# Performance work log

Hardware: AMD Instinct MI355X
Metric: run time of the kernel (lower is better)

## Reference

```python
import jax, jax.numpy as jnp
import numpy as np

N_NODES = 100000
N_EDGES = 1600000
D_FEAT = 64


def setup_inputs() -> dict:
    key = jax.random.key(0)
    k1, k2 = jax.random.split(key)
    x = jax.random.normal(k1, (N_NODES, D_FEAT), dtype=jnp.float32)
    edge_index = jax.random.randint(k2, (2, N_EDGES), 0, N_NODES, dtype=jnp.int64)
    alpha = jnp.ones((), dtype=jnp.float32)
    res_scale = jnp.ones((), dtype=jnp.float32)
    return {"x": x, "alpha": alpha, "res_scale": res_scale, "edge_index": edge_index}


def reference(x, alpha, res_scale, edge_index):
    """LGConv (symmetric gcn_norm, no self-loops) -> alpha-scale -> residual.

    out_i = alpha * sum_{(j->i) in E} x_j / sqrt(deg_i * deg_j) + res_scale * x_i
    """
    n = x.shape[0]
    row, col = edge_index[0], edge_index[1]  # source, target
    # degree from target index (as in PyG gcn_norm with add_self_loops=False)
    deg = jax.ops.segment_sum(jnp.ones(row.shape[0], dtype=x.dtype), col, num_segments=n)
    deg_inv_sqrt = jnp.where(deg > 0, jax.lax.rsqrt(jnp.maximum(deg, 1.0)), 0.0)
    norm = deg_inv_sqrt[row] * deg_inv_sqrt[col]  # (E,)
    msgs = norm[:, None] * x[row]                  # (E, d) gather + scale
    out = jax.ops.segment_sum(msgs, col, num_segments=n)  # scatter-add to targets
    return alpha * out + res_scale * x
```

## Files before the change

### kernel.cpp

```cpp
#include <hip/hip_runtime.h>
#include <hip/hip_bf16.h>

#define D_FEAT 64
#define OVF_CAP 65536
#define EB 4096
#define NBMAX 1024

typedef unsigned int uint32;

__device__ inline float blo(uint32 u) { return __uint_as_float(u << 16); }
__device__ inline float bhi(uint32 u) { return __uint_as_float(u & 0xffff0000u); }
__device__ inline float dinv(int d) { return (d > 0) ? rsqrtf((float)d) : 0.0f; }

__global__ __launch_bounds__(1024) void k_scatter(const int* __restrict__ row,
                                                  const int* __restrict__ col,
                                                  const float2* __restrict__ x2,
                                                  uint32* __restrict__ xb,
                                                  int* __restrict__ deg,
                                                  int* __restrict__ cursor,
                                                  uint32* __restrict__ binned,
                                                  int* __restrict__ slots,
                                                  int2* __restrict__ ovf,
                                                  int* __restrict__ ovf_cnt,
                                                  int nhalf, int E, int nb,
                                                  int CAP, int C) {
    __shared__ int h[NBMAX];
    for (int i = threadIdx.x; i < nb; i += 1024) h[i] = 0;
    __syncthreads();
    const int s = blockIdx.x * EB;
    const int e = (s + EB < E) ? s + EB : E;
    for (int i = s + threadIdx.x; i < e; i += 1024)
        atomicAdd(&h[col[i] >> 7], 1);
    __syncthreads();
    for (int k = threadIdx.x; k < nb; k += 1024) {
        int c = h[k];
        if (c) h[k] = atomicAdd(&cursor[k], c);
    }
    __syncthreads();
    for (int i = s + threadIdx.x; i < e; i += 1024) {
        int c = col[i];
        uint32 r = (uint32)row[i];
        int b = c >> 7;
        int pos = atomicAdd(&h[b], 1);
        if (pos < CAP) {
            binned[(size_t)b * CAP + pos] = (r << 7) | (uint32)(c & 127);
        } else {
            int rk = atomicAdd(&deg[c], 1);
            if (rk < C) {
                slots[(size_t)c * C + rk] = (int)r;
            } else {
                int o = atomicAdd(ovf_cnt, 1);
                if (o < OVF_CAP) ovf[o] = make_int2((int)r, c);
            }
        }
    }
    const int t = blockIdx.x * 1024 + threadIdx.x;
    const int stride = gridDim.x * 1024;
    for (int j = t; j < nhalf; j += stride) {
        float2 v = x2[j];
        __hip_bfloat16 bx = __float2bfloat16(v.x);
        __hip_bfloat16 by = __float2bfloat16(v.y);
        uint32 ux = *reinterpret_cast<unsigned short*>(&bx);
        uint32 uy = *reinterpret_cast<unsigned short*>(&by);
        xb[j] = ux | (uy << 16);
    }
}

__global__ __launch_bounds__(512) void k_build(const int* __restrict__ cursor,
                                               const uint32* __restrict__ binned,
                                               int* __restrict__ slots,
                                               int* __restrict__ deg,
                                               float* __restrict__ winv,
                                               int2* __restrict__ ovf,
                                               int* __restrict__ ovf_cnt,
                                               int n, int C, int CAP) {
    __shared__ int cnt[128];
    const int k = blockIdx.x;
    const int base = k << 7;
    if (threadIdx.x < 128) {
        int node = base + threadIdx.x;
        cnt[threadIdx.x] = (node < n) ? deg[node] : 0;
    }
    __syncthreads();
    int tot = cursor[k];
    const int e = (tot < CAP) ? tot : CAP;
    const uint32* seg = binned + (size_t)k * CAP;
    for (int i = threadIdx.x; i < e; i += 512) {
        uint32 pk = seg[i];
        int cl = (int)(pk & 127);
        int r  = (int)(pk >> 7);
        int rk = atomicAdd(&cnt[cl], 1);
        if (rk < C) {
            slots[(size_t)(base + cl) * C + rk] = r;
        } else {
            int o = atomicAdd(ovf_cnt, 1);
            if (o < OVF_CAP) ovf[o] = make_int2(r, base + cl);
        }
    }
    __syncthreads();
    int i = base + threadIdx.x;
    if (threadIdx.x < 128 && i < n) {
        int d = cnt[threadIdx.x];
        deg[i] = d;
        winv[i] = dinv(d);
    }
}

__global__ void k_gather4d(const uint32* __restrict__ xb,
                           const float4* __restrict__ x4,
                           const int* __restrict__ deg,
                           const float* __restrict__ winv,
                           const int* __restrict__ slots,
                           const float* __restrict__ alpha_p,
                           const float* __restrict__ rs_p,
                           float4* __restrict__ out4, int n, int C) {
    int wid = (blockIdx.x * blockDim.x + threadIdx.x) >> 6;
    if (wid >= n) return;
    const int lane = threadIdx.x & 63;
    const int q = lane >> 4;
    const int l = lane & 15;
    int d = deg[wid];
    int e = (d < C) ? d : C;
    float4 xr = make_float4(0.f, 0.f, 0.f, 0.f);
    if (q == 0) xr = x4[(size_t)wid * 16 + l];
    const int* sl = slots + (size_t)wid * C;
    float ax = 0.f, ay = 0.f, az = 0.f, aw = 0.f;
    int k = 0;
    for (; k + 16 <= e; k += 16) {
        int s0 = sl[k + q];
        int s1 = sl[k + 4 + q];
        int s2 = sl[k + 8 + q];
        int s3 = sl[k + 12 + q];
        float w0 = winv[s0], w1 = winv[s1], w2 = winv[s2], w3 = winv[s3];
        uint2 p0 = ((const uint2*)(xb + (size_t)s0 * 32))[l];
        uint2 p1 = ((const uint2*)(xb + (size_t)s1 * 32))[l];
        uint2 p2 = ((const uint2*)(xb + (size_t)s2 * 32))[l];
        uint2 p3 = ((const uint2*)(xb + (size_t)s3 * 32))[l];
        ax = fmaf(w0, blo(p0.x), ax); ay = fmaf(w0, bhi(p0.x), ay);
        az = fmaf(w0, blo(p0.y), az); aw = fmaf(w0, bhi(p0.y), aw);
        ax = fmaf(w1, blo(p1.x), ax); ay = fmaf(w1, bhi(p1.x), ay);
        az = fmaf(w1, blo(p1.y), az); aw = fmaf(w1, bhi(p1.y), aw);
        ax = fmaf(w2, blo(p2.x), ax); ay = fmaf(w2, bhi(p2.x), ay);
        az = fmaf(w2, blo(p2.y), az); aw = fmaf(w2, bhi(p2.y), aw);
        ax = fmaf(w3, blo(p3.x), ax); ay = fmaf(w3, bhi(p3.x), ay);
        az = fmaf(w3, blo(p3.y), az); aw = fmaf(w3, bhi(p3.y), aw);
    }
    for (; k < e; k += 4) {
        int kk = k + q;
        if (kk < e) {
            int s0 = sl[kk];
            float w0 = winv[s0];
            uint2 p0 = ((const uint2*)(xb + (size_t)s0 * 32))[l];
            ax = fmaf(w0, blo(p0.x), ax); ay = fmaf(w0, bhi(p0.x), ay);
            az = fmaf(w0, blo(p0.y), az); aw = fmaf(w0, bhi(p0.y), aw);
        }
    }
    ax += __shfl_down(ax, 32, 64); ay += __shfl_down(ay, 32, 64);
    az += __shfl_down(az, 32, 64); aw += __shfl_down(aw, 32, 64);
    ax += __shfl_down(ax, 16, 64); ay += __shfl_down(ay, 16, 64);
    az += __shfl_down(az, 16, 64); aw += __shfl_down(aw, 16, 64);
    if (q == 0) {
        float adw = (*alpha_p) * winv[wid];
        float rs  = *rs_p;
        float4 o;
        o.x = fmaf(adw, ax, rs * xr.x);
        o.y = fmaf(adw, ay, rs * xr.y);
        o.z = fmaf(adw, az, rs * xr.z);
        o.w = fmaf(adw, aw, rs * xr.w);
        out4[(size_t)wid * 16 + l] = o;
    }
}

__global__ void k_ovf(const int2* __restrict__ ovf, const int* __restrict__ cnt_p,
                      const float* __restrict__ x, const float* __restrict__ winv,
                      const float* __restrict__ alpha_p, float* __restrict__ out) {
    int cnt = *cnt_p;
    if (cnt > OVF_CAP) cnt = OVF_CAP;
    if (cnt <= 0) return;
    float a = *alpha_p;
    long long total = (long long)cnt * 64;
    long long stride = (long long)gridDim.x * blockDim.x;
    for (long long idx = blockIdx.x * (long long)blockDim.x + threadIdx.x;
         idx < total; idx += stride) {
        int e = (int)(idx >> 6);
        int f = (int)(idx & 63);
        int2 rc = ovf[e];
        float w = a * winv[rc.x] * winv[rc.y];
        atomicAdd(&out[(size_t)rc.y * D_FEAT + f], w * x[(size_t)rc.x * D_FEAT + f]);
    }
}

__global__ void k_winv(const int* __restrict__ deg, float* __restrict__ winv, int n) {
    int i = blockIdx.x * blockDim.x + threadIdx.x;
    if (i < n) winv[i] = dinv(deg[i]);
}

__global__ __launch_bounds__(256) void k_prep(const float2* __restrict__ x2,
                                              uint32* __restrict__ xb,
                                              const int* __restrict__ row,
                                              const int* __restrict__ col,
                                              int* __restrict__ deg,
                                              int* __restrict__ slots,
                                              int2* __restrict__ ovf,
                                              int* __restrict__ ovf_cnt,
                                              int nhalf, int E, int C) {
    const int t = blockIdx.x * blockDim.x + threadIdx.x;
    if (t < E) {
        int c = col[t];
        int r = row[t];
        int rk = atomicAdd(&deg[c], 1);
        if (rk < C) {
            slots[(size_t)c * C + rk] = r;
        } else {
            int o = atomicAdd(ovf_cnt, 1);
            if (o < OVF_CAP) ovf[o] = make_int2(r, c);
        }
    }
    const int stride = gridDim.x * blockDim.x;
    for (int j = t; j < nhalf; j += stride) {
        float2 v = x2[j];
        __hip_bfloat16 bx = __float2bfloat16(v.x);
        __hip_bfloat16 by = __float2bfloat16(v.y);
        uint32 ux = *reinterpret_cast<unsigned short*>(&bx);
        uint32 uy = *reinterpret_cast<unsigned short*>(&by);
        xb[j] = ux | (uy << 16);
    }
}

static inline char* align_up(char* p, size_t a) {
    return (char*)(((uintptr_t)p + (a - 1)) & ~(uintptr_t)(a - 1));
}

extern "C" void kernel_launch(void* const* d_in, const int* in_sizes, int n_in,
                              void* d_out, int out_size, void* d_ws, size_t ws_size,
                              hipStream_t stream) {
    const float* x         = (const float*)d_in[0];
    const float* alpha     = (const float*)d_in[1];
    const float* res_scale = (const float*)d_in[2];
    const int*   ei        = (const int*)d_in[3];

    const int n = in_sizes[0] / D_FEAT;
    const int E = in_sizes[3] / 2;
    const int* row = ei;
    const int* col = ei + E;

    float* out = (float*)d_out;
    const int nhalf = n * (D_FEAT / 2);
    const int nb = (n + 127) >> 7;
    const int B  = (E + EB - 1) / EB;
    const int C  = 32;

    {
        char* p = (char*)d_ws;
        int*    deg     = (int*)p;            p += (size_t)n * 4;
        int*    cursor  = (int*)p;            p += (size_t)nb * 4;
        int*    ovf_cnt = (int*)p;            p += 4;
        float*  winv    = (float*)p;          p += (size_t)n * 4;
        int2*   ovf     = (int2*)p;           p += (size_t)OVF_CAP * 8;
        p = align_up(p, 16);
        uint32* xb      = (uint32*)p;         p += (size_t)n * 128;
        int*    slots   = (int*)p;            p += (size_t)n * C * 4;
        p = align_up(p, 16);
        uint32* binned  = (uint32*)p;
        const size_t fixed = (size_t)((char*)binned - (char*)d_ws);

        int CAP = 0;
        if (ws_size > fixed) {
            long long avail = (long long)(ws_size - fixed) / ((long long)nb * 4);
            CAP = (avail > 4096) ? 4096 : (int)avail;
            CAP &= ~31;
        }
        const bool ok = (CAP >= 1600) && (nb <= NBMAX) && (n <= (NBMAX << 7));
        if (ok) {
            hipMemsetAsync(deg, 0, (size_t)(n + nb + 1) * 4, stream);
            k_scatter<<<B, 1024, 0, stream>>>(row, col, (const float2*)x, xb,
                                              deg, cursor, binned, slots,
                                              ovf, ovf_cnt, nhalf, E, nb, CAP, C);
            k_build<<<nb, 512, 0, stream>>>(cursor, binned, slots, deg, winv,
                                            ovf, ovf_cnt, n, C, CAP);
            const long long tt = (long long)n * D_FEAT;
            const int blocks = (int)((tt + 255) / 256);
            k_gather4d<<<blocks, 256, 0, stream>>>(xb, (const float4*)x, deg, winv,
                                                   slots, alpha, res_scale,
                                                   (float4*)out, n, C);
            k_ovf<<<64, 256, 0, stream>>>(ovf, ovf_cnt, x, winv, alpha, out);
            return;
        }
    }

    {
        char* q = (char*)d_ws;
        int*    degf    = (int*)q;            q += (size_t)n * 4;
        int*    ovf_cf  = (int*)q;            q += 4;
        float*  winvf   = (float*)q;          q += (size_t)n * 4;
        int2*   ovff    = (int2*)q;           q += (size_t)OVF_CAP * 8;
        q = align_up(q, 16);
        uint32* xbf     = (uint32*)q;         q += (size_t)n * 128;
        int*    slotsf  = (int*)q;
        const size_t fxd = (size_t)(q - (char*)d_ws);
        int Cf = 0;
        if (ws_size > fxd) {
            size_t c_avail = (ws_size - fxd) / ((size_t)n * 4);
            Cf = (c_avail > 32) ? 32 : (int)c_avail;
        }
        if (Cf < 1) return;
        hipMemsetAsync(degf, 0, (size_t)n * 4 + 4, stream);
        k_prep<<<(E + 255) / 256, 256, 0, stream>>>(
            (const float2*)x, xbf, row, col, degf, slotsf, ovff, ovf_cf,
            nhalf, E, Cf);
        k_winv<<<(n + 255) / 256, 256, 0, stream>>>(degf, winvf, n);
        const long long tt = (long long)n * D_FEAT;
        const int blocks = (int)((tt + 255) / 256);
        k_gather4d<<<blocks, 256, 0, stream>>>(xbf, (const float4*)x, degf, winvf,
                                               slotsf, alpha, res_scale,
                                               (float4*)out, n, Cf);
        k_ovf<<<64, 256, 0, stream>>>(ovff, ovf_cf, x, winvf, alpha, out);
    }
}
```

Measured before the change: 182.4 us.

## Fuse scatter, build and gather into one cooperative kernel with LDS slot lists

Replaces the separate scatter, build and gather kernels with one cooperative kernel that uses grid-wide syncs between phases. Each block owns 128 target nodes and keeps their neighbor slot lists in shared memory rather than a global slots array, which removes the global slot writes and reads and two kernel launches. Binning now runs on only 256 blocks with larger edge chunks. The cost is grid.sync overhead, occupancy limited to one block per 128 nodes (782 blocks), and lower parallelism in the binning phase.

```diff
diff --git a/kernel.cpp b/kernel.cpp
--- a/kernel.cpp
+++ b/kernel.cpp
@@ -1,10 +1,14 @@
 #include <hip/hip_runtime.h>
 #include <hip/hip_bf16.h>
+#include <hip/hip_cooperative_groups.h>
+
+namespace cg = cooperative_groups;
 
 #define D_FEAT 64
 #define OVF_CAP 65536
-#define EB 4096
+#define NBIN 256
 #define NBMAX 1024
+#define CSLOT 32
 
 typedef unsigned int uint32;
 
@@ -12,50 +16,201 @@
 __device__ inline float bhi(uint32 u) { return __uint_as_float(u & 0xffff0000u); }
 __device__ inline float dinv(int d) { return (d > 0) ? rsqrtf((float)d) : 0.0f; }
 
-__global__ __launch_bounds__(1024) void k_scatter(const int* __restrict__ row,
-                                                  const int* __restrict__ col,
-                                                  const float2* __restrict__ x2,
-                                                  uint32* __restrict__ xb,
-                                                  int* __restrict__ deg,
-                                                  int* __restrict__ cursor,
-                                                  uint32* __restrict__ binned,
-                                                  int* __restrict__ slots,
-                                                  int2* __restrict__ ovf,
-                                                  int* __restrict__ ovf_cnt,
-                                                  int nhalf, int E, int nb,
-                                                  int CAP, int C) {
-    __shared__ int h[NBMAX];
-    for (int i = threadIdx.x; i < nb; i += 1024) h[i] = 0;
-    __syncthreads();
-    const int s = blockIdx.x * EB;
-    const int e = (s + EB < E) ? s + EB : E;
-    for (int i = s + threadIdx.x; i < e; i += 1024)
-        atomicAdd(&h[col[i] >> 7], 1);
-    __syncthreads();
-    for (int k = threadIdx.x; k < nb; k += 1024) {
-        int c = h[k];
-        if (c) h[k] = atomicAdd(&cursor[k], c);
-    }
-    __syncthreads();
-    for (int i = s + threadIdx.x; i < e; i += 1024) {
-        int c = col[i];
-        uint32 r = (uint32)row[i];
-        int b = c >> 7;
-        int pos = atomicAdd(&h[b], 1);
-        if (pos < CAP) {
-            binned[(size_t)b * CAP + pos] = (r << 7) | (uint32)(c & 127);
-        } else {
-            int rk = atomicAdd(&deg[c], 1);
-            if (rk < C) {
-                slots[(size_t)c * C + rk] = (int)r;
+__global__ __launch_bounds__(512, 8) void k_coop(
+    const int* __restrict__ row, const int* __restrict__ col,
+    const float2* __restrict__ x2, uint32* __restrict__ xb,
+    int* __restrict__ deg, float* __restrict__ winv,
+    int* __restrict__ cursor, uint32* __restrict__ binned,
+    int2* __restrict__ ovf, int* __restrict__ ovf_cnt,
+    const float* __restrict__ alpha_p, const float* __restrict__ rs_p,
+    const float4* __restrict__ x4, float4* __restrict__ out4,
+    int n, int E, int nb, int CAP, int EB2, int nhalf)
+{
+    __shared__ int   slots[128 * CSLOT];
+    __shared__ int   cnt[128];
+    __shared__ float winvl[128];
+    const int bid = blockIdx.x;
+    const int tid = threadIdx.x;
+    cg::grid_group grid = cg::this_grid();
+
+    if (bid < NBIN) {
+        int* h = slots;
+        for (int i = tid; i < nb; i += 512) h[i] = 0;
+        __syncthreads();
+        const int s = bid * EB2;
+        const int e = (s + EB2 < E) ? s + EB2 : E;
+        for (int i = s + tid; i < e; i += 512)
+            atomicAdd(&h[col[i] >> 7], 1);
+        __syncthreads();
+        for (int k = tid; k < nb; k += 512) {
+            int c = h[k];
+            if (c) h[k] = atomicAdd(&cursor[k], c);
+        }
+        __syncthreads();
+        for (int i = s + tid; i < e; i += 512) {
+            int c = col[i];
+            uint32 r = (uint32)row[i];
+            int b = c >> 7;
+            int pos = atomicAdd(&h[b], 1);
+            if (pos < CAP) {
+                binned[(size_t)b * CAP + pos] = (r << 7) | (uint32)(c & 127);
             } else {
+                atomicAdd(&deg[c], 1);
                 int o = atomicAdd(ovf_cnt, 1);
                 if (o < OVF_CAP) ovf[o] = make_int2((int)r, c);
             }
         }
     }
-    const int t = blockIdx.x * 1024 + threadIdx.x;
-    const int stride = gridDim.x * 1024;
+    for (int j = bid * 512 + tid; j < nhalf; j += nb * 512) {
+        float2 v = x2[j];
+        __hip_bfloat16 bx = __float2bfloat16(v.x);
+        __hip_bfloat16 by = __float2bfloat16(v.y);
+        uint32 ux = *reinterpret_cast<unsigned short*>(&bx);
+        uint32 uy = *reinterpret_cast<unsigned short*>(&by);
+        xb[j] = ux | (uy << 16);
+    }
+    grid.sync();
+
+    if (tid < 128) cnt[tid] = 0;
+    __syncthreads();
+    const int base = bid << 7;
+    int tot = cursor[bid];
+    if (tot > CAP) tot = CAP;
+    const uint32* seg = binned + (size_t)bid * CAP;
+    for (int i = tid; i < tot; i += 512) {
+        uint32 pk = seg[i];
+        int cl = (int)(pk & 127);
+        int r  = (int)(pk >> 7);
+        int rk = atomicAdd(&cnt[cl], 1);
+        if (rk < CSLOT) {
+            slots[(cl << 5) + rk] = r;
+        } else {
+            int o = atomicAdd(ovf_cnt, 1);
+            if (o < OVF_CAP) ovf[o] = make_int2(r, base + cl);
+        }
+    }
+    __syncthreads();
+    if (tid < 128) {
+        int node = base + tid;
+        if (node < n) {
+            int d = cnt[tid] + deg[node];
+            deg[node] = d;
+            float w = dinv(d);
+            winv[node] = w;
+            winvl[tid] = w;
+        } else {
+            winvl[tid] = 0.f;
+        }
+    }
+    grid.sync();
+
+    const int wv   = tid >> 6;
+    const int lane = tid & 63;
+    const int q = lane >> 4;
+    const int l = lane & 15;
+    const float alpha = *alpha_p;
+    const float rs = *rs_p;
+    for (int nl = (wv << 4); nl < (wv << 4) + 16; ++nl) {
+        int node = base + nl;
+        if (node >= n) break;
+        int e = cnt[nl];
+        if (e > CSLOT) e = CSLOT;
+        float4 xr = make_float4(0.f, 0.f, 0.f, 0.f);
+        if (q == 0) xr = x4[(size_t)node * 16 + l];
+        const int* sl = &slots[nl << 5];
+        float ax = 0.f, ay = 0.f, az = 0.f, aw = 0.f;
+        int k = 0;
+        for (; k + 16 <= e; k += 16) {
+            int s0 = sl[k + q];
+            int s1 = sl[k + 4 + q];
+            int s2 = sl[k + 8 + q];
+            int s3 = sl[k + 12 + q];
+            float w0 = winv[s0], w1 = winv[s1], w2 = winv[s2], w3 = winv[s3];
+            uint2 p0 = ((const uint2*)(xb + (size_t)s0 * 32))[l];
+            uint2 p1 = ((const uint2*)(xb + (size_t)s1 * 32))[l];
+            uint2 p2 = ((const uint2*)(xb + (size_t)s2 * 32))[l];
+            uint2 p3 = ((const uint2*)(xb + (size_t)s3 * 32))[l];
+            ax = fmaf(w0, blo(p0.x), ax); ay = fmaf(w0, bhi(p0.x), ay);
+            az = fmaf(w0, blo(p0.y), az); aw = fmaf(w0, bhi(p0.y), aw);
+            ax = fmaf(w1, blo(p1.x), ax); ay = fmaf(w1, bhi(p1.x), ay);
+            az = fmaf(w1, blo(p1.y), az); aw = fmaf(w1, bhi(p1.y), aw);
+            ax = fmaf(w2, blo(p2.x), ax); ay = fmaf(w2, bhi(p2.x), ay);
+            az = fmaf(w2, blo(p2.y), az); aw = fmaf(w2, bhi(p2.y), aw);
+            ax = fmaf(w3, blo(p3.x), ax); ay = fmaf(w3, bhi(p3.x), ay);
+            az = fmaf(w3, blo(p3.y), az); aw = fmaf(w3, bhi(p3.y), aw);
+        }
+        for (; k < e; k += 4) {
+            int kk = k + q;
+            if (kk < e) {
+                int s0 = sl[kk];
+                float w0 = winv[s0];
+                uint2 p0 = ((const uint2*)(xb + (size_t)s0 * 32))[l];
+                ax = fmaf(w0, blo(p0.x), ax); ay = fmaf(w0, bhi(p0.x), ay);
+                az = fmaf(w0, blo(p0.y), az); aw = fmaf(w0, bhi(p0.y), aw);
+            }
+        }
+        ax += __shfl_down(ax, 32, 64); ay += __shfl_down(ay, 32, 64);
+        az += __shfl_down(az, 32, 64); aw += __shfl_down(aw, 32, 64);
+        ax += __shfl_down(ax, 16, 64); ay += __shfl_down(ay, 16, 64);
+        az += __shfl_down(az, 16, 64); aw += __shfl_down(aw, 16, 64);
+        if (q == 0) {
+            float adw = alpha * winvl[nl];
+            float4 o;
+            o.x = fmaf(adw, ax, rs * xr.x);
+            o.y = fmaf(adw, ay, rs * xr.y);
+            o.z = fmaf(adw, az, rs * xr.z);
+            o.w = fmaf(adw, aw, rs * xr.w);
+            out4[(size_t)node * 16 + l] = o;
+        }
+    }
+}
+
+__global__ void k_ovf(const int2* __restrict__ ovf, const int* __restrict__ cnt_p,
+                      const float* __restrict__ x, const float* __restrict__ winv,
+                      const float* __restrict__ alpha_p, float* __restrict__ out) {
+    int cnt = *cnt_p;
+    if (cnt > OVF_CAP) cnt = OVF_CAP;
+    if (cnt <= 0) return;
+    float a = *alpha_p;
+    long long total = (long long)cnt * 64;
+    long long stride = (long long)gridDim.x * blockDim.x;
+    for (long long idx = blockIdx.x * (long long)blockDim.x + threadIdx.x;
+         idx < total; idx += stride) {
+        int e = (int)(idx >> 6);
+        int f = (int)(idx & 63);
+        int2 rc = ovf[e];
+        float w = a * winv[rc.x] * winv[rc.y];
+        atomicAdd(&out[(size_t)rc.y * D_FEAT + f], w * x[(size_t)rc.x * D_FEAT + f]);
+    }
+}
+
+__global__ void k_winv(const int* __restrict__ deg, float* __restrict__ winv, int n) {
+    int i = blockIdx.x * blockDim.x + threadIdx.x;
+    if (i < n) winv[i] = dinv(deg[i]);
+}
+
+__global__ __launch_bounds__(256) void k_prep(const float2* __restrict__ x2,
+                                              uint32* __restrict__ xb,
+                                              const int* __restrict__ row,
+                                              const int* __restrict__ col,
+                                              int* __restrict__ deg,
+                                              int* __restrict__ slots,
+                                              int2* __restrict__ ovf,
+                                              int* __restrict__ ovf_cnt,
+                                              int nhalf, int E, int C) {
+    const int t = blockIdx.x * blockDim.x + threadIdx.x;
+    if (t < E) {
+        int c = col[t];
+        int r = row[t];
+        int rk = atomicAdd(&deg[c], 1);
+        if (rk < C) {
+            slots[(size_t)c * C + rk] = r;
+        } else {
+            int o = atomicAdd(ovf_cnt, 1);
+            if (o < OVF_CAP) ovf[o] = make_int2(r, c);
+        }
+    }
+    const int stride = gridDim.x * blockDim.x;
     for (int j = t; j < nhalf; j += stride) {
         float2 v = x2[j];
         __hip_bfloat16 bx = __float2bfloat16(v.x);
@@ -63,46 +218,6 @@
         uint32 ux = *reinterpret_cast<unsigned short*>(&bx);
         uint32 uy = *reinterpret_cast<unsigned short*>(&by);
         xb[j] = ux | (uy << 16);
-    }
-}
-
-__global__ __launch_bounds__(512) void k_build(const int* __restrict__ cursor,
-                                               const uint32* __restrict__ binned,
-                                               int* __restrict__ slots,
-                                               int* __restrict__ deg,
-                                               float* __restrict__ winv,
-                                               int2* __restrict__ ovf,
-                                               int* __restrict__ ovf_cnt,
-                                               int n, int C, int CAP) {
-    __shared__ int cnt[128];
-    const int k = blockIdx.x;
-    const int base = k << 7;
-    if (threadIdx.x < 128) {
-        int node = base + threadIdx.x;
-        cnt[threadIdx.x] = (node < n) ? deg[node] : 0;
-    }
-    __syncthreads();
-    int tot = cursor[k];
-    const int e = (tot < CAP) ? tot : CAP;
-    const uint32* seg = binned + (size_t)k * CAP;
-    for (int i = threadIdx.x; i < e; i += 512) {
-        uint32 pk = seg[i];
-        int cl = (int)(pk & 127);
-        int r  = (int)(pk >> 7);
-        int rk = atomicAdd(&cnt[cl], 1);
-        if (rk < C) {
-            slots[(size_t)(base + cl) * C + rk] = r;
-        } else {
-            int o = atomicAdd(ovf_cnt, 1);
-            if (o < OVF_CAP) ovf[o] = make_int2(r, base + cl);
-        }
-    }
-    __syncthreads();
-    int i = base + threadIdx.x;
-    if (threadIdx.x < 128 && i < n) {
-        int d = cnt[threadIdx.x];
-        deg[i] = d;
-        winv[i] = dinv(d);
     }
 }
 
@@ -171,62 +286,6 @@
     }
 }
 
-__global__ void k_ovf(const int2* __restrict__ ovf, const int* __restrict__ cnt_p,
-                      const float* __restrict__ x, const float* __restrict__ winv,
-                      const float* __restrict__ alpha_p, float* __restrict__ out) {
-    int cnt = *cnt_p;
-    if (cnt > OVF_CAP) cnt = OVF_CAP;
-    if (cnt <= 0) return;
-    float a = *alpha_p;
-    long long total = (long long)cnt * 64;
-    long long stride = (long long)gridDim.x * blockDim.x;
-    for (long long idx = blockIdx.x * (long long)blockDim.x + threadIdx.x;
-         idx < total; idx += stride) {
-        int e = (int)(idx >> 6);
-        int f = (int)(idx & 63);
-        int2 rc = ovf[e];
-        float w = a * winv[rc.x] * winv[rc.y];
-        atomicAdd(&out[(size_t)rc.y * D_FEAT + f], w * x[(size_t)rc.x * D_FEAT + f]);
-    }
-}
-
-__global__ void k_winv(const int* __restrict__ deg, float* __restrict__ winv, int n) {
-    int i = blockIdx.x * blockDim.x + threadIdx.x;
-    if (i < n) winv[i] = dinv(deg[i]);
-}
-
-__global__ __launch_bounds__(256) void k_prep(const float2* __restrict__ x2,
-                                              uint32* __restrict__ xb,
-                                              const int* __restrict__ row,
-                                              const int* __restrict__ col,
-                                              int* __restrict__ deg,
-                                              int* __restrict__ slots,
-                                              int2* __restrict__ ovf,
-                                              int* __restrict__ ovf_cnt,
-                                              int nhalf, int E, int C) {
-    const int t = blockIdx.x * blockDim.x + threadIdx.x;
-    if (t < E) {
-        int c = col[t];
-        int r = row[t];
-        int rk = atomicAdd(&deg[c], 1);
-        if (rk < C) {
-            slots[(size_t)c * C + rk] = r;
-        } else {
-            int o = atomicAdd(ovf_cnt, 1);
-            if (o < OVF_CAP) ovf[o] = make_int2(r, c);
-        }
-    }
-    const int stride = gridDim.x * blockDim.x;
-    for (int j = t; j < nhalf; j += stride) {
-        float2 v = x2[j];
-        __hip_bfloat16 bx = __float2bfloat16(v.x);
-        __hip_bfloat16 by = __float2bfloat16(v.y);
-        uint32 ux = *reinterpret_cast<unsigned short*>(&bx);
-        uint32 uy = *reinterpret_cast<unsigned short*>(&by);
-        xb[j] = ux | (uy << 16);
-    }
-}
-
 static inline char* align_up(char* p, size_t a) {
     return (char*)(((uintptr_t)p + (a - 1)) & ~(uintptr_t)(a - 1));
 }
@@ -247,8 +306,7 @@
     float* out = (float*)d_out;
     const int nhalf = n * (D_FEAT / 2);
     const int nb = (n + 127) >> 7;
-    const int B  = (E + EB - 1) / EB;
-    const int C  = 32;
+    const int EB2 = (E + NBIN - 1) / NBIN;
 
     {
         char* p = (char*)d_ws;
@@ -259,7 +317,6 @@
         int2*   ovf     = (int2*)p;           p += (size_t)OVF_CAP * 8;
         p = align_up(p, 16);
         uint32* xb      = (uint32*)p;         p += (size_t)n * 128;
-        int*    slots   = (int*)p;            p += (size_t)n * C * 4;
         p = align_up(p, 16);
         uint32* binned  = (uint32*)p;
         const size_t fixed = (size_t)((char*)binned - (char*)d_ws);
@@ -270,21 +327,44 @@
             CAP = (avail > 4096) ? 4096 : (int)avail;
             CAP &= ~31;
         }
-        const bool ok = (CAP >= 1600) && (nb <= NBMAX) && (n <= (NBMAX << 7));
+
+        static int coop_cap = -1;
+        if (coop_cap < 0) {
+            int perCU = 0, nCU = 0, dev = 0;
+            hipGetDevice(&dev);
+            if (hipOccupancyMaxActiveBlocksPerMultiprocessor(&perCU, k_coop,
+                                                             512, 0) != hipSuccess)
+                perCU = 0;
+            if (hipDeviceGetAttribute(&nCU, hipDeviceAttributeMultiprocessorCount,
+                                      dev) != hipSuccess)
+                nCU = 0;
+            coop_cap = perCU * nCU;
+        }
+
+        const bool ok = (CAP >= 2560) && (nb <= NBMAX) && (nb <= coop_cap);
         if (ok) {
             hipMemsetAsync(deg, 0, (size_t)(n + nb + 1) * 4, stream);
-            k_scatter<<<B, 1024, 0, stream>>>(row, col, (const float2*)x, xb,
-                                              deg, cursor, binned, slots,
-                                              ovf, ovf_cnt, nhalf, E, nb, CAP, C);
-            k_build<<<nb, 512, 0, stream>>>(cursor, binned, slots, deg, winv,
-                                            ovf, ovf_cnt, n, C, CAP);
-            const long long tt = (long long)n * D_FEAT;
-            const int blocks = (int)((tt + 255) / 256);
-            k_gather4d<<<blocks, 256, 0, stream>>>(xb, (const float4*)x, deg, winv,
-                                                   slots, alpha, res_scale,
-                                                   (float4*)out, n, C);
-            k_ovf<<<64, 256, 0, stream>>>(ovf, ovf_cnt, x, winv, alpha, out);
-            return;
+            const int*    row_a = row;      const int*   col_a = col;
+            const float2* x2_a  = (const float2*)x;
+            uint32*       xb_a  = xb;       int*         deg_a = deg;
+            float*        wv_a  = winv;     int*         cur_a = cursor;
+            uint32*       bin_a = binned;   int2*        ovf_a = ovf;
+            int*          ovc_a = ovf_cnt;
+            const float*  al_a  = alpha;    const float* rs_a  = res_scale;
+            const float4* x4_a  = (const float4*)x;
+            float4*       out_a = (float4*)out;
+            int n_a = n, E_a = E, nb_a = nb, CAP_a = CAP, EB2_a = EB2,
+                nh_a = nhalf;
+            void* args[] = { &row_a, &col_a, &x2_a, &xb_a, &deg_a, &wv_a,
+                             &cur_a, &bin_a, &ovf_a, &ovc_a, &al_a, &rs_a,
+                             &x4_a, &out_a, &n_a, &E_a, &nb_a, &CAP_a,
+                             &EB2_a, &nh_a };
+            hipError_t err = hipLaunchCooperativeKernel(
+                (const void*)k_coop, dim3(nb), dim3(512), args, 0, stream);
+            if (err == hipSuccess) {
+                k_ovf<<<64, 256, 0, stream>>>(ovf, ovf_cnt, x, winv, alpha, out);
+                return;
+            }
         }
     }
 
```

Result: slower. 247.3 us (+35.6%).

## Replace atomic binning with two-pass ballot-based radix partition and in-place slot ranking

Applied to the files above, without the earlier changes.

The one-pass scatter kernel used per-edge shared-memory atomics to sort edges into 128-node bins. It is replaced by a two-level radix partition: first by 4096-node range, then into 32 sub-bins. Each level uses wave ballot and popcount prefix sums instead of atomics. A rank kernel stages each bin in LDS and writes per-node slot lists back into the binned buffer in place, so the separate slots array is gone. The range buffer reuses the bf16 x storage before it is written. This adds an extra kernel pass and heavy unrolled ballot loops over 32 buckets. It also depends on tight capacity assumptions such as n ≤ 131072 and the per-bin cap CAPB.

```diff
diff --git a/kernel.cpp b/kernel.cpp
--- a/kernel.cpp
+++ b/kernel.cpp
@@ -3,106 +3,219 @@
 
 #define D_FEAT 64
 #define OVF_CAP 65536
-#define EB 4096
-#define NBMAX 1024
+#define NRMAX 32
+#define RS_EB 2048
+#define NCH 16
+#define CAPB 4096
+#define CSL 32
 
 typedef unsigned int uint32;
+typedef unsigned long long ull;
 
 __device__ inline float blo(uint32 u) { return __uint_as_float(u << 16); }
 __device__ inline float bhi(uint32 u) { return __uint_as_float(u & 0xffff0000u); }
 __device__ inline float dinv(int d) { return (d > 0) ? rsqrtf((float)d) : 0.0f; }
 
-__global__ __launch_bounds__(1024) void k_scatter(const int* __restrict__ row,
-                                                  const int* __restrict__ col,
-                                                  const float2* __restrict__ x2,
-                                                  uint32* __restrict__ xb,
-                                                  int* __restrict__ deg,
-                                                  int* __restrict__ cursor,
-                                                  uint32* __restrict__ binned,
-                                                  int* __restrict__ slots,
-                                                  int2* __restrict__ ovf,
-                                                  int* __restrict__ ovf_cnt,
-                                                  int nhalf, int E, int nb,
-                                                  int CAP, int C) {
-    __shared__ int h[NBMAX];
-    for (int i = threadIdx.x; i < nb; i += 1024) h[i] = 0;
+__global__ __launch_bounds__(256) void k_rsplit(const int* __restrict__ row,
+                                                const int* __restrict__ col,
+                                                uint32* __restrict__ rseg,
+                                                int* __restrict__ rcur,
+                                                int* __restrict__ deg,
+                                                int2* __restrict__ ovf,
+                                                int* __restrict__ ovf_cnt,
+                                                int E, int nr, int RCAP) {
+    __shared__ int wcnt[4][NRMAX];
+    __shared__ int wbase[4][NRMAX];
+    const int wv = threadIdx.x >> 6;
+    const int lane = threadIdx.x & 63;
+    const ull mlt = ((ull)1 << lane) - 1;
+    const int s = blockIdx.x * RS_EB;
+
+    int cnt[NRMAX];
+#pragma unroll
+    for (int k = 0; k < NRMAX; ++k) cnt[k] = 0;
+#pragma unroll
+    for (int it = 0; it < RS_EB / 256; ++it) {
+        int i = s + it * 256 + wv * 64 + lane;
+        int b = 63;
+        if (i < E) b = col[i] >> 12;
+#pragma unroll
+        for (int k = 0; k < NRMAX; ++k)
+            cnt[k] += __popcll(__ballot(b == k));
+    }
+    if (lane == 0) {
+#pragma unroll
+        for (int k = 0; k < NRMAX; ++k) wcnt[wv][k] = cnt[k];
+    }
     __syncthreads();
-    const int s = blockIdx.x * EB;
-    const int e = (s + EB < E) ? s + EB : E;
-    for (int i = s + threadIdx.x; i < e; i += 1024)
-        atomicAdd(&h[col[i] >> 7], 1);
+    if (threadIdx.x < NRMAX) {
+        int k = threadIdx.x;
+        int t0 = wcnt[0][k], t1 = wcnt[1][k], t2 = wcnt[2][k], t3 = wcnt[3][k];
+        int tot = t0 + t1 + t2 + t3;
+        int g = tot ? atomicAdd(&rcur[k], tot) : 0;
+        wbase[0][k] = g;
+        wbase[1][k] = g + t0;
+        wbase[2][k] = g + t0 + t1;
+        wbase[3][k] = g + t0 + t1 + t2;
+    }
     __syncthreads();
-    for (int k = threadIdx.x; k < nb; k += 1024) {
-        int c = h[k];
-        if (c) h[k] = atomicAdd(&cursor[k], c);
-    }
+    int run[NRMAX];
+#pragma unroll
+    for (int k = 0; k < NRMAX; ++k) run[k] = wbase[wv][k];
+#pragma unroll
+    for (int it = 0; it < RS_EB / 256; ++it) {
+        int i = s + it * 256 + wv * 64 + lane;
+        int b = 63, c = 0, r = 0;
+        if (i < E) { c = col[i]; r = row[i]; b = c >> 12; }
+#pragma unroll
+        for (int k = 0; k < NRMAX; ++k) {
+            ull m = __ballot(b == k);
+            if (b == k) {
+                int pos = run[k] + __popcll(m & mlt);
+                if (pos < RCAP) {
+                    rseg[(size_t)k * RCAP + pos] =
+                        ((uint32)r << 12) | (uint32)(c & 4095);
+                } else {
+                    atomicAdd(&deg[c], 1);
+                    int o = atomicAdd(ovf_cnt, 1);
+                    if (o < OVF_CAP) ovf[o] = make_int2(r, c);
+                }
+            }
+            run[k] += __popcll(m);
+        }
+    }
+}
+
+__global__ __launch_bounds__(512) void k_bsplit(const uint32* __restrict__ rseg,
+                                                const int* __restrict__ rcur,
+                                                uint32* __restrict__ binned,
+                                                int* __restrict__ cursor,
+                                                int* __restrict__ deg,
+                                                int2* __restrict__ ovf,
+                                                int* __restrict__ ovf_cnt,
+                                                int nr, int RCAP) {
+    __shared__ int wcnt[8][32];
+    __shared__ int wbase[8][32];
+    const int rg = blockIdx.x & 31;
+    if (rg >= nr) return;
+    int len = rcur[rg];
+    if (len > RCAP) len = RCAP;
+    const uint32* sg = rseg + (size_t)rg * RCAP;
+    const int wv = threadIdx.x >> 6;
+    const int lane = threadIdx.x & 63;
+    const ull mlt = ((ull)1 << lane) - 1;
+
+    for (int c0 = (blockIdx.x >> 5) * 4096; c0 < len; c0 += NCH * 4096) {
+        const int cend = (c0 + 4096 < len) ? c0 + 4096 : len;
+        int cnt[32];
+#pragma unroll
+        for (int k = 0; k < 32; ++k) cnt[k] = 0;
+#pragma unroll
+        for (int it = 0; it < 8; ++it) {
+            int i = c0 + it * 512 + wv * 64 + lane;
+            int b = 63;
+            if (i < cend) b = (int)((sg[i] >> 7) & 31);
+#pragma unroll
+            for (int k = 0; k < 32; ++k)
+                cnt[k] += __popcll(__ballot(b == k));
+        }
+        if (lane == 0) {
+#pragma unroll
+            for (int k = 0; k < 32; ++k) wcnt[wv][k] = cnt[k];
+        }
+        __syncthreads();
+        if (threadIdx.x < 32) {
+            int k = threadIdx.x;
+            int tot = 0, acc;
+            int t[8];
+#pragma unroll
+            for (int w = 0; w < 8; ++w) { t[w] = wcnt[w][k]; tot += t[w]; }
+            int g = tot ? atomicAdd(&cursor[(rg << 5) + k], tot) : 0;
+            acc = g;
+#pragma unroll
+            for (int w = 0; w < 8; ++w) { wbase[w][k] = acc; acc += t[w]; }
+        }
+        __syncthreads();
+        int run[32];
+#pragma unroll
+        for (int k = 0; k < 32; ++k) run[k] = wbase[wv][k];
+#pragma unroll
+        for (int it = 0; it < 8; ++it) {
+            int i = c0 + it * 512 + wv * 64 + lane;
+            int b = 63;
+            uint32 v = 0;
+            if (i < cend) { v = sg[i]; b = (int)((v >> 7) & 31); }
+#pragma unroll
+            for (int k = 0; k < 32; ++k) {
+                ull m = __ballot(b == k);
+                if (b == k) {
+                    int pos = run[k] + __popcll(m & mlt);
+                    int bk = (rg << 5) + k;
+                    if (pos < CAPB) {
+                        binned[(size_t)bk * CAPB + pos] =
+                            ((v >> 12) << 7) | (v & 127u);
+                    } else {
+                        int cf = (rg << 12) + (int)(v & 4095u);
+                        atomicAdd(&deg[cf], 1);
+                        int o = atomicAdd(ovf_cnt, 1);
+                        if (o < OVF_CAP) ovf[o] = make_int2((int)(v >> 12), cf);
+                    }
+                }
+                run[k] += __popcll(m);
+            }
+        }
+        __syncthreads();
+    }
+}
+
+__global__ __launch_bounds__(512) void k_rank(const int* __restrict__ cursor,
+                                              uint32* __restrict__ binned,
+                                              int* __restrict__ deg,
+                                              float* __restrict__ winv,
+                                              const float2* __restrict__ x2,
+                                              uint32* __restrict__ xb,
+                                              int2* __restrict__ ovf,
+                                              int* __restrict__ ovf_cnt,
+                                              int n, int nbk, int nhalf) {
+    __shared__ uint32 sh[CAPB];
+    __shared__ int cnt[128];
+    const int bid = blockIdx.x;
+    int tot = cursor[bid];
+    if (tot > CAPB) tot = CAPB;
+    uint32* win = binned + (size_t)bid * CAPB;
+    for (int i = threadIdx.x; i < tot; i += 512) sh[i] = win[i];
+    if (threadIdx.x < 128) cnt[threadIdx.x] = 0;
     __syncthreads();
-    for (int i = s + threadIdx.x; i < e; i += 1024) {
-        int c = col[i];
-        uint32 r = (uint32)row[i];
-        int b = c >> 7;
-        int pos = atomicAdd(&h[b], 1);
-        if (pos < CAP) {
-            binned[(size_t)b * CAP + pos] = (r << 7) | (uint32)(c & 127);
+    const int base = bid << 7;
+    for (int i = threadIdx.x; i < tot; i += 512) {
+        uint32 pk = sh[i];
+        int cl = (int)(pk & 127);
+        int r  = (int)(pk >> 7);
+        int rk = atomicAdd(&cnt[cl], 1);
+        if (rk < CSL) {
+            win[(cl << 5) + rk] = (uint32)r;
         } else {
-            int rk = atomicAdd(&deg[c], 1);
-            if (rk < C) {
-                slots[(size_t)c * C + rk] = (int)r;
-            } else {
-                int o = atomicAdd(ovf_cnt, 1);
-                if (o < OVF_CAP) ovf[o] = make_int2((int)r, c);
-            }
-        }
-    }
-    const int t = blockIdx.x * 1024 + threadIdx.x;
-    const int stride = gridDim.x * 1024;
-    for (int j = t; j < nhalf; j += stride) {
+            int o = atomicAdd(ovf_cnt, 1);
+            if (o < OVF_CAP) ovf[o] = make_int2(r, base + cl);
+        }
+    }
+    __syncthreads();
+    if (threadIdx.x < 128) {
+        int node = base + threadIdx.x;
+        if (node < n) {
+            int sc = cnt[threadIdx.x];
+            int dtrue = deg[node] + sc;
+            winv[node] = dinv(dtrue);
+            deg[node] = sc;
+        }
+    }
+    for (int j = bid * 512 + threadIdx.x; j < nhalf; j += nbk * 512) {
         float2 v = x2[j];
         __hip_bfloat16 bx = __float2bfloat16(v.x);
         __hip_bfloat16 by = __float2bfloat16(v.y);
         uint32 ux = *reinterpret_cast<unsigned short*>(&bx);
         uint32 uy = *reinterpret_cast<unsigned short*>(&by);
         xb[j] = ux | (uy << 16);
-    }
-}
-
-__global__ __launch_bounds__(512) void k_build(const int* __restrict__ cursor,
-                                               const uint32* __restrict__ binned,
-                                               int* __restrict__ slots,
-                                               int* __restrict__ deg,
-                                               float* __restrict__ winv,
-                                               int2* __restrict__ ovf,
-                                               int* __restrict__ ovf_cnt,
-                                               int n, int C, int CAP) {
-    __shared__ int cnt[128];
-    const int k = blockIdx.x;
-    const int base = k << 7;
-    if (threadIdx.x < 128) {
-        int node = base + threadIdx.x;
-        cnt[threadIdx.x] = (node < n) ? deg[node] : 0;
-    }
-    __syncthreads();
-    int tot = cursor[k];
-    const int e = (tot < CAP) ? tot : CAP;
-    const uint32* seg = binned + (size_t)k * CAP;
-    for (int i = threadIdx.x; i < e; i += 512) {
-        uint32 pk = seg[i];
-        int cl = (int)(pk & 127);
-        int r  = (int)(pk >> 7);
-        int rk = atomicAdd(&cnt[cl], 1);
-        if (rk < C) {
-            slots[(size_t)(base + cl) * C + rk] = r;
-        } else {
-            int o = atomicAdd(ovf_cnt, 1);
-            if (o < OVF_CAP) ovf[o] = make_int2(r, base + cl);
-        }
-    }
-    __syncthreads();
-    int i = base + threadIdx.x;
-    if (threadIdx.x < 128 && i < n) {
-        int d = cnt[threadIdx.x];
-        deg[i] = d;
-        winv[i] = dinv(d);
     }
 }
 
@@ -246,43 +359,43 @@
 
     float* out = (float*)d_out;
     const int nhalf = n * (D_FEAT / 2);
-    const int nb = (n + 127) >> 7;
-    const int B  = (E + EB - 1) / EB;
-    const int C  = 32;
+    const int nr  = (n + 4095) >> 12;
+    const int nbk = nr << 5;
 
     {
         char* p = (char*)d_ws;
         int*    deg     = (int*)p;            p += (size_t)n * 4;
-        int*    cursor  = (int*)p;            p += (size_t)nb * 4;
+        int*    cursor  = (int*)p;            p += (size_t)(NRMAX * 32) * 4;
+        int*    rcur    = (int*)p;            p += NRMAX * 4;
         int*    ovf_cnt = (int*)p;            p += 4;
         float*  winv    = (float*)p;          p += (size_t)n * 4;
         int2*   ovf     = (int2*)p;           p += (size_t)OVF_CAP * 8;
         p = align_up(p, 16);
         uint32* xb      = (uint32*)p;         p += (size_t)n * 128;
-        int*    slots   = (int*)p;            p += (size_t)n * C * 4;
         p = align_up(p, 16);
-        uint32* binned  = (uint32*)p;
-        const size_t fixed = (size_t)((char*)binned - (char*)d_ws);
-
-        int CAP = 0;
-        if (ws_size > fixed) {
-            long long avail = (long long)(ws_size - fixed) / ((long long)nb * 4);
-            CAP = (avail > 4096) ? 4096 : (int)avail;
-            CAP &= ~31;
-        }
-        const bool ok = (CAP >= 1600) && (nb <= NBMAX) && (n <= (NBMAX << 7));
+        uint32* binned  = (uint32*)p;         p += (size_t)nbk * CAPB * 4;
+        const size_t need = (size_t)(p - (char*)d_ws);
+
+        uint32* rseg = xb;
+        const int RCAP = (int)(((size_t)n * 128 / 4) / nr);
+
+        const bool ok = (nr <= NRMAX) && (n <= (1 << 17)) &&
+                        (RCAP >= E / nr + 8192) && (need <= ws_size);
         if (ok) {
-            hipMemsetAsync(deg, 0, (size_t)(n + nb + 1) * 4, stream);
-            k_scatter<<<B, 1024, 0, stream>>>(row, col, (const float2*)x, xb,
-                                              deg, cursor, binned, slots,
-                                              ovf, ovf_cnt, nhalf, E, nb, CAP, C);
-            k_build<<<nb, 512, 0, stream>>>(cursor, binned, slots, deg, winv,
-                                            ovf, ovf_cnt, n, C, CAP);
+            hipMemsetAsync(deg, 0, (size_t)(n + NRMAX * 32 + NRMAX + 1) * 4, stream);
+            const int B1 = (E + RS_EB - 1) / RS_EB;
+            k_rsplit<<<B1, 256, 0, stream>>>(row, col, rseg, rcur, deg,
+                                             ovf, ovf_cnt, E, nr, RCAP);
+            k_bsplit<<<32 * NCH, 512, 0, stream>>>(rseg, rcur, binned, cursor,
+                                                   deg, ovf, ovf_cnt, nr, RCAP);
+            k_rank<<<nbk, 512, 0, stream>>>(cursor, binned, deg, winv,
+                                            (const float2*)x, xb, ovf, ovf_cnt,
+                                            n, nbk, nhalf);
             const long long tt = (long long)n * D_FEAT;
             const int blocks = (int)((tt + 255) / 256);
             k_gather4d<<<blocks, 256, 0, stream>>>(xb, (const float4*)x, deg, winv,
-                                                   slots, alpha, res_scale,
-                                                   (float4*)out, n, C);
+                                                   (const int*)binned, alpha,
+                                                   res_scale, (float4*)out, n, CSL);
             k_ovf<<<64, 256, 0, stream>>>(ovf, ovf_cnt, x, winv, alpha, out);
             return;
         }
```

New measurement: 265.3 us. +45.5%, slower.

## Build per-bucket adjacency in LDS and fuse with gather, pre-scale bf16 features

Applied to the files above, without the earlier changes.

Replaces the global slots array and the separate build kernel with a bucketed gather kernel. Each block reads its binned edges, builds per-node neighbor lists in shared memory and immediately accumulates neighbor features. Degrees are now counted with global atomics during binning. A new cast kernel folds the source-side inverse-sqrt degree into the bf16 copy of x, so the gather no longer applies a per-edge weight. This removes the global slot write and re-read, but adds per-edge global atomics and runs the gather on fewer, larger blocks that each walk 16 nodes per wave serially.

```diff
diff --git a/kernel.cpp b/kernel.cpp
--- a/kernel.cpp
+++ b/kernel.cpp
@@ -5,6 +5,8 @@
 #define OVF_CAP 65536
 #define EB 4096
 #define NBMAX 1024
+#define CAPB 4096
+#define CSL 32
 
 typedef unsigned int uint32;
 
@@ -12,25 +14,24 @@
 __device__ inline float bhi(uint32 u) { return __uint_as_float(u & 0xffff0000u); }
 __device__ inline float dinv(int d) { return (d > 0) ? rsqrtf((float)d) : 0.0f; }
 
-__global__ __launch_bounds__(1024) void k_scatter(const int* __restrict__ row,
-                                                  const int* __restrict__ col,
-                                                  const float2* __restrict__ x2,
-                                                  uint32* __restrict__ xb,
-                                                  int* __restrict__ deg,
-                                                  int* __restrict__ cursor,
-                                                  uint32* __restrict__ binned,
-                                                  int* __restrict__ slots,
-                                                  int2* __restrict__ ovf,
-                                                  int* __restrict__ ovf_cnt,
-                                                  int nhalf, int E, int nb,
-                                                  int CAP, int C) {
+__global__ __launch_bounds__(1024) void k_bin(const int* __restrict__ row,
+                                              const int* __restrict__ col,
+                                              int* __restrict__ deg,
+                                              int* __restrict__ cursor,
+                                              uint32* __restrict__ binned,
+                                              int2* __restrict__ ovf,
+                                              int* __restrict__ ovf_cnt,
+                                              int E, int nb) {
     __shared__ int h[NBMAX];
     for (int i = threadIdx.x; i < nb; i += 1024) h[i] = 0;
     __syncthreads();
     const int s = blockIdx.x * EB;
     const int e = (s + EB < E) ? s + EB : E;
-    for (int i = s + threadIdx.x; i < e; i += 1024)
-        atomicAdd(&h[col[i] >> 7], 1);
+    for (int i = s + threadIdx.x; i < e; i += 1024) {
+        int c = col[i];
+        atomicAdd(&h[c >> 7], 1);
+        atomicAdd(&deg[c], 1);
+    }
     __syncthreads();
     for (int k = threadIdx.x; k < nb; k += 1024) {
         int c = h[k];
@@ -42,20 +43,177 @@
         uint32 r = (uint32)row[i];
         int b = c >> 7;
         int pos = atomicAdd(&h[b], 1);
-        if (pos < CAP) {
-            binned[(size_t)b * CAP + pos] = (r << 7) | (uint32)(c & 127);
+        if (pos < CAPB) {
+            binned[(size_t)b * CAPB + pos] = (r << 7) | (uint32)(c & 127);
         } else {
-            int rk = atomicAdd(&deg[c], 1);
-            if (rk < C) {
-                slots[(size_t)c * C + rk] = (int)r;
-            } else {
-                int o = atomicAdd(ovf_cnt, 1);
-                if (o < OVF_CAP) ovf[o] = make_int2((int)r, c);
+            int o = atomicAdd(ovf_cnt, 1);
+            if (o < OVF_CAP) ovf[o] = make_int2((int)r, c);
+        }
+    }
+}
+
+__global__ __launch_bounds__(256) void k_wcast(const int* __restrict__ deg,
+                                               float* __restrict__ winv,
+                                               const float2* __restrict__ x2,
+                                               uint32* __restrict__ xb,
+                                               int n, int nhalf) {
+    const int t = blockIdx.x * 256 + threadIdx.x;
+    const int stride = gridDim.x * 256;
+    for (int i = t; i < n; i += stride) winv[i] = dinv(deg[i]);
+    for (int j = t; j < nhalf; j += stride) {
+        int node = j >> 5;
+        float w = dinv(deg[node]);
+        float2 v = x2[j];
+        __hip_bfloat16 bx = __float2bfloat16(v.x * w);
+        __hip_bfloat16 by = __float2bfloat16(v.y * w);
+        uint32 ux = *reinterpret_cast<unsigned short*>(&bx);
+        uint32 uy = *reinterpret_cast<unsigned short*>(&by);
+        xb[j] = ux | (uy << 16);
+    }
+}
+
+__global__ __launch_bounds__(512) void k_rgather(const int* __restrict__ cursor,
+                                                 const uint32* __restrict__ binned,
+                                                 const float* __restrict__ winv,
+                                                 const uint32* __restrict__ xb,
+                                                 const float4* __restrict__ x4,
+                                                 const float* __restrict__ alpha_p,
+                                                 const float* __restrict__ rs_p,
+                                                 float4* __restrict__ out4,
+                                                 int2* __restrict__ ovf,
+                                                 int* __restrict__ ovf_cnt,
+                                                 int n) {
+    __shared__ int   slots[128 * CSL];
+    __shared__ int   cnt[128];
+    __shared__ float winvl[128];
+    const int bid = blockIdx.x;
+    const int tid = threadIdx.x;
+    if (tid < 128) cnt[tid] = 0;
+    __syncthreads();
+    const int base = bid << 7;
+    int tot = cursor[bid];
+    if (tot > CAPB) tot = CAPB;
+    const uint32* seg = binned + (size_t)bid * CAPB;
+    for (int i = tid; i < tot; i += 512) {
+        uint32 pk = seg[i];
+        int cl = (int)(pk & 127);
+        int r  = (int)(pk >> 7);
+        int rk = atomicAdd(&cnt[cl], 1);
+        if (rk < CSL) {
+            slots[(cl << 5) + rk] = r;
+        } else {
+            int o = atomicAdd(ovf_cnt, 1);
+            if (o < OVF_CAP) ovf[o] = make_int2(r, base + cl);
+        }
+    }
+    __syncthreads();
+    if (tid < 128) {
+        int node = base + tid;
+        winvl[tid] = (node < n) ? winv[node] : 0.f;
+    }
+    __syncthreads();
+
+    const int wv   = tid >> 6;
+    const int lane = tid & 63;
+    const int q = lane >> 4;
+    const int l = lane & 15;
+    const float alpha = *alpha_p;
+    const float rs = *rs_p;
+    for (int nl = (wv << 4); nl < (wv << 4) + 16; ++nl) {
+        int node = base + nl;
+        if (node >= n) break;
+        int e = cnt[nl];
+        if (e > CSL) e = CSL;
+        float4 xr = make_float4(0.f, 0.f, 0.f, 0.f);
+        if (q == 0) xr = x4[(size_t)node * 16 + l];
+        const int* sl = &slots[nl << 5];
+        float ax = 0.f, ay = 0.f, az = 0.f, aw = 0.f;
+        int k = 0;
+        for (; k + 16 <= e; k += 16) {
+            int s0 = sl[k + q];
+            int s1 = sl[k + 4 + q];
+            int s2 = sl[k + 8 + q];
+            int s3 = sl[k + 12 + q];
+            uint2 p0 = ((const uint2*)(xb + (size_t)s0 * 32))[l];
+            uint2 p1 = ((const uint2*)(xb + (size_t)s1 * 32))[l];
+            uint2 p2 = ((const uint2*)(xb + (size_t)s2 * 32))[l];
+            uint2 p3 = ((const uint2*)(xb + (size_t)s3 * 32))[l];
+            ax += blo(p0.x); ay += bhi(p0.x); az += blo(p0.y); aw += bhi(p0.y);
+            ax += blo(p1.x); ay += bhi(p1.x); az += blo(p1.y); aw += bhi(p1.y);
+            ax += blo(p2.x); ay += bhi(p2.x); az += blo(p2.y); aw += bhi(p2.y);
+            ax += blo(p3.x); ay += bhi(p3.x); az += blo(p3.y); aw += bhi(p3.y);
+        }
+        for (; k < e; k += 4) {
+            int kk = k + q;
+            if (kk < e) {
+                int s0 = sl[kk];
+                uint2 p0 = ((const uint2*)(xb + (size_t)s0 * 32))[l];
+                ax += blo(p0.x); ay += bhi(p0.x);
+                az += blo(p0.y); aw += bhi(p0.y);
             }
         }
-    }
-    const int t = blockIdx.x * 1024 + threadIdx.x;
-    const int stride = gridDim.x * 1024;
+        ax += __shfl_down(ax, 32, 64); ay += __shfl_down(ay, 32, 64);
+        az += __shfl_down(az, 32, 64); aw += __shfl_down(aw, 32, 64);
+        ax += __shfl_down(ax, 16, 64); ay += __shfl_down(ay, 16, 64);
+        az += __shfl_down(az, 16, 64); aw += __shfl_down(aw, 16, 64);
+        if (q == 0) {
+            float adw = alpha * winvl[nl];
+            float4 o;
+            o.x = fmaf(adw, ax, rs * xr.x);
+            o.y = fmaf(adw, ay, rs * xr.y);
+            o.z = fmaf(adw, az, rs * xr.z);
+            o.w = fmaf(adw, aw, rs * xr.w);
+            out4[(size_t)node * 16 + l] = o;
+        }
+    }
+}
+
+__global__ void k_ovf(const int2* __restrict__ ovf, const int* __restrict__ cnt_p,
+                      const float* __restrict__ x, const float* __restrict__ winv,
+                      const float* __restrict__ alpha_p, float* __restrict__ out) {
+    int cnt = *cnt_p;
+    if (cnt > OVF_CAP) cnt = OVF_CAP;
+    if (cnt <= 0) return;
+    float a = *alpha_p;
+    long long total = (long long)cnt * 64;
+    long long stride = (long long)gridDim.x * blockDim.x;
+    for (long long idx = blockIdx.x * (long long)blockDim.x + threadIdx.x;
+         idx < total; idx += stride) {
+        int e = (int)(idx >> 6);
+        int f = (int)(idx & 63);
+        int2 rc = ovf[e];
+        float w = a * winv[rc.x] * winv[rc.y];
+        atomicAdd(&out[(size_t)rc.y * D_FEAT + f], w * x[(size_t)rc.x * D_FEAT + f]);
+    }
+}
+
+__global__ void k_winv(const int* __restrict__ deg, float* __restrict__ winv, int n) {
+    int i = blockIdx.x * blockDim.x + threadIdx.x;
+    if (i < n) winv[i] = dinv(deg[i]);
+}
+
+__global__ __launch_bounds__(256) void k_prep(const float2* __restrict__ x2,
+                                              uint32* __restrict__ xb,
+                                              const int* __restrict__ row,
+                                              const int* __restrict__ col,
+                                              int* __restrict__ deg,
+                                              int* __restrict__ slots,
+                                              int2* __restrict__ ovf,
+                                              int* __restrict__ ovf_cnt,
+                                              int nhalf, int E, int C) {
+    const int t = blockIdx.x * blockDim.x + threadIdx.x;
+    if (t < E) {
+        int c = col[t];
+        int r = row[t];
+        int rk = atomicAdd(&deg[c], 1);
+        if (rk < C) {
+            slots[(size_t)c * C + rk] = r;
+        } else {
+            int o = atomicAdd(ovf_cnt, 1);
+            if (o < OVF_CAP) ovf[o] = make_int2(r, c);
+        }
+    }
+    const int stride = gridDim.x * blockDim.x;
     for (int j = t; j < nhalf; j += stride) {
         float2 v = x2[j];
         __hip_bfloat16 bx = __float2bfloat16(v.x);
@@ -63,46 +221,6 @@
         uint32 ux = *reinterpret_cast<unsigned short*>(&bx);
         uint32 uy = *reinterpret_cast<unsigned short*>(&by);
         xb[j] = ux | (uy << 16);
-    }
-}
-
-__global__ __launch_bounds__(512) void k_build(const int* __restrict__ cursor,
-                                               const uint32* __restrict__ binned,
-                                               int* __restrict__ slots,
-                                               int* __restrict__ deg,
-                                               float* __restrict__ winv,
-                                               int2* __restrict__ ovf,
-                                               int* __restrict__ ovf_cnt,
-                                               int n, int C, int CAP) {
-    __shared__ int cnt[128];
-    const int k = blockIdx.x;
-    const int base = k << 7;
-    if (threadIdx.x < 128) {
-        int node = base + threadIdx.x;
-        cnt[threadIdx.x] = (node < n) ? deg[node] : 0;
-    }
-    __syncthreads();
-    int tot = cursor[k];
-    const int e = (tot < CAP) ? tot : CAP;
-    const uint32* seg = binned + (size_t)k * CAP;
-    for (int i = threadIdx.x; i < e; i += 512) {
-        uint32 pk = seg[i];
-        int cl = (int)(pk & 127);
-        int r  = (int)(pk >> 7);
-        int rk = atomicAdd(&cnt[cl], 1);
-        if (rk < C) {
-            slots[(size_t)(base + cl) * C + rk] = r;
-        } else {
-            int o = atomicAdd(ovf_cnt, 1);
-            if (o < OVF_CAP) ovf[o] = make_int2(r, base + cl);
-        }
-    }
-    __syncthreads();
-    int i = base + threadIdx.x;
-    if (threadIdx.x < 128 && i < n) {
-        int d = cnt[threadIdx.x];
-        deg[i] = d;
-        winv[i] = dinv(d);
     }
 }
 
@@ -171,62 +289,6 @@
     }
 }
 
-__global__ void k_ovf(const int2* __restrict__ ovf, const int* __restrict__ cnt_p,
-                      const float* __restrict__ x, const float* __restrict__ winv,
-                      const float* __restrict__ alpha_p, float* __restrict__ out) {
-    int cnt = *cnt_p;
-    if (cnt > OVF_CAP) cnt = OVF_CAP;
-    if (cnt <= 0) return;
-    float a = *alpha_p;
-    long long total = (long long)cnt * 64;
-    long long stride = (long long)gridDim.x * blockDim.x;
-    for (long long idx = blockIdx.x * (long long)blockDim.x + threadIdx.x;
-         idx < total; idx += stride) {
-        int e = (int)(idx >> 6);
-        int f = (int)(idx & 63);
-        int2 rc = ovf[e];
-        float w = a * winv[rc.x] * winv[rc.y];
-        atomicAdd(&out[(size_t)rc.y * D_FEAT + f], w * x[(size_t)rc.x * D_FEAT + f]);
-    }
-}
-
-__global__ void k_winv(const int* __restrict__ deg, float* __restrict__ winv, int n) {
-    int i = blockIdx.x * blockDim.x + threadIdx.x;
-    if (i < n) winv[i] = dinv(deg[i]);
-}
-
-__global__ __launch_bounds__(256) void k_prep(const float2* __restrict__ x2,
-                                              uint32* __restrict__ xb,
-                                              const int* __restrict__ row,
-                                              const int* __restrict__ col,
-                                              int* __restrict__ deg,
-                                              int* __restrict__ slots,
-                                              int2* __restrict__ ovf,
-                                              int* __restrict__ ovf_cnt,
-                                              int nhalf, int E, int C) {
-    const int t = blockIdx.x * blockDim.x + threadIdx.x;
-    if (t < E) {
-        int c = col[t];
-        int r = row[t];
-        int rk = atomicAdd(&deg[c], 1);
-        if (rk < C) {
-            slots[(size_t)c * C + rk] = r;
-        } else {
-            int o = atomicAdd(ovf_cnt, 1);
-            if (o < OVF_CAP) ovf[o] = make_int2(r, c);
-        }
-    }
-    const int stride = gridDim.x * blockDim.x;
-    for (int j = t; j < nhalf; j += stride) {
-        float2 v = x2[j];
-        __hip_bfloat16 bx = __float2bfloat16(v.x);
-        __hip_bfloat16 by = __float2bfloat16(v.y);
-        uint32 ux = *reinterpret_cast<unsigned short*>(&bx);
-        uint32 uy = *reinterpret_cast<unsigned short*>(&by);
-        xb[j] = ux | (uy << 16);
-    }
-}
-
 static inline char* align_up(char* p, size_t a) {
     return (char*)(((uintptr_t)p + (a - 1)) & ~(uintptr_t)(a - 1));
 }
@@ -247,8 +309,7 @@
     float* out = (float*)d_out;
     const int nhalf = n * (D_FEAT / 2);
     const int nb = (n + 127) >> 7;
-    const int B  = (E + EB - 1) / EB;
-    const int C  = 32;
+    const int B1 = (E + EB - 1) / EB;
 
     {
         char* p = (char*)d_ws;
@@ -259,30 +320,22 @@
         int2*   ovf     = (int2*)p;           p += (size_t)OVF_CAP * 8;
         p = align_up(p, 16);
         uint32* xb      = (uint32*)p;         p += (size_t)n * 128;
-        int*    slots   = (int*)p;            p += (size_t)n * C * 4;
         p = align_up(p, 16);
-        uint32* binned  = (uint32*)p;
-        const size_t fixed = (size_t)((char*)binned - (char*)d_ws);
-
-        int CAP = 0;
-        if (ws_size > fixed) {
-            long long avail = (long long)(ws_size - fixed) / ((long long)nb * 4);
-            CAP = (avail > 4096) ? 4096 : (int)avail;
-            CAP &= ~31;
-        }
-        const bool ok = (CAP >= 1600) && (nb <= NBMAX) && (n <= (NBMAX << 7));
+        uint32* binned  = (uint32*)p;         p += (size_t)nb * CAPB * 4;
+        const size_t need = (size_t)(p - (char*)d_ws);
+
+        const bool ok = (need <= ws_size) && (nb <= NBMAX) && (n <= (NBMAX << 7));
         if (ok) {
             hipMemsetAsync(deg, 0, (size_t)(n + nb + 1) * 4, stream);
-            k_scatter<<<B, 1024, 0, stream>>>(row, col, (const float2*)x, xb,
-                                              deg, cursor, binned, slots,
-                                              ovf, ovf_cnt, nhalf, E, nb, CAP, C);
-            k_build<<<nb, 512, 0, stream>>>(cursor, binned, slots, deg, winv,
-                                            ovf, ovf_cnt, n, C, CAP);
-            const long long tt = (long long)n * D_FEAT;
-            const int blocks = (int)((tt + 255) / 256);
-            k_gather4d<<<blocks, 256, 0, stream>>>(xb, (const float4*)x, deg, winv,
-                                                   slots, alpha, res_scale,
-                                                   (float4*)out, n, C);
+            k_bin<<<B1, 1024, 0, stream>>>(row, col, deg, cursor, binned,
+                                           ovf, ovf_cnt, E, nb);
+            int wblocks = (nhalf + 255) / 256;
+            if (wblocks > 1024) wblocks = 1024;
+            k_wcast<<<wblocks, 256, 0, stream>>>(deg, winv, (const float2*)x, xb,
+                                                 n, nhalf);
+            k_rgather<<<nb, 512, 0, stream>>>(cursor, binned, winv, xb,
+                                              (const float4*)x, alpha, res_scale,
+                                              (float4*)out, ovf, ovf_cnt, n);
             k_ovf<<<64, 256, 0, stream>>>(ovf, ovf_cnt, x, winv, alpha, out);
             return;
         }
```

Result: slower. 223.4 us (+22.5%).
